# Kernel tuning notes

Hardware: AMD Instinct MI355X
Metric: run time of the kernel (lower is better)

The kernel has to match this reference:

```python
import jax, jax.numpy as jnp
import numpy as np

EMBED_DIM = 2048
HEAD_DIM = 128            # __init__ head_dim arg
HALF = HEAD_DIM // 2      # internal self.head_dim = 64
NH2 = EMBED_DIM // HALF   # 32 q/k heads
H = NH2 // 2              # 16 differential heads
DEPTH = 12
LAMBDA_INIT = 0.8 - 0.6 * float(np.exp(-0.3 * DEPTH))
SCALING = HEAD_DIM ** (-0.5)   # source divides scores by this (== *sqrt(head_dim))
BATCH, SEQ = 1, 2048
EPS = 1e-5


def setup_inputs() -> dict:
    key = jax.random.key(0)
    ks = jax.random.split(key, 10)
    wstd = 0.25 / float(np.sqrt(EMBED_DIM))  # keep logits moderate despite *sqrt(head_dim)
    return {
        "x": jax.random.normal(ks[0], (BATCH, SEQ, EMBED_DIM), jnp.float32),
        "wq": jax.random.normal(ks[1], (EMBED_DIM, EMBED_DIM), jnp.float32) * wstd,
        "wk": jax.random.normal(ks[2], (EMBED_DIM, EMBED_DIM), jnp.float32) * wstd,
        "wv": jax.random.normal(ks[3], (EMBED_DIM, EMBED_DIM), jnp.float32) * wstd,
        "wout": jax.random.normal(ks[4], (EMBED_DIM, EMBED_DIM), jnp.float32) * wstd,
        "lambda_q1": jax.random.normal(ks[5], (HALF,), jnp.float32) * 0.1,
        "lambda_q2": jax.random.normal(ks[6], (HALF,), jnp.float32) * 0.1,
        "lambda_k1": jax.random.normal(ks[7], (HALF,), jnp.float32) * 0.1,
        "lambda_k2": jax.random.normal(ks[8], (HALF,), jnp.float32) * 0.1,
        "subln_weight": jnp.ones((2 * HALF,), jnp.float32),
    }


def _rope_tables(t, dim):
    # precompute_freqs_cis: freqs = 1/theta^(arange(0,dim,2)/dim); angles = outer(t, freqs)
    inv = 1.0 / (10000.0 ** (np.arange(0, dim, 2)[: dim // 2].astype(np.float64) / dim))
    ang = np.outer(np.arange(t), inv)
    return jnp.asarray(np.cos(ang), jnp.float32), jnp.asarray(np.sin(ang), jnp.float32)


def _apply_rope(x, cos, sin):
    # x: [b, t, h, d]; interleaved (even, odd) pairs form complex numbers
    xr, xi = x[..., 0::2], x[..., 1::2]
    c = cos[None, :, None, :]
    s = sin[None, :, None, :]
    out = jnp.stack([xr * c - xi * s, xr * s + xi * c], axis=-1)
    return out.reshape(x.shape)


def reference(x, wq, wk, wv, wout, lambda_q1, lambda_q2, lambda_k1, lambda_k2, subln_weight):
    b, t, e = x.shape
    # nn.Linear(bias=False): y = x @ W^T
    q = (x @ wq.T).reshape(b, t, NH2, HALF)
    k = (x @ wk.T).reshape(b, t, NH2, HALF)
    v = (x @ wv.T).reshape(b, t, H, 2 * HALF)  # intended DIFF-attn layout
    cos, sin = _rope_tables(t, HALF)
    q = _apply_rope(q, cos, sin)
    k = _apply_rope(k, cos, sin)
    q = q.transpose(0, 2, 1, 3)  # [b, 2H, t, HALF]
    k = k.transpose(0, 2, 1, 3)
    v = v.transpose(0, 2, 1, 3)  # [b, H, t, 2*HALF]
    # source: attn_weights = qk / scaling  (scaling = head_dim**-0.5 -> multiply by sqrt(head_dim))
    scores = jnp.einsum('bhtd,bhsd->bhts', q, k) / SCALING
    # default attn_mask = triu(zeros) == all zeros -> no masking applied
    probs = jax.nn.softmax(scores, axis=-1)
    lam1 = jnp.exp(jnp.sum(lambda_q1 * lambda_k1))
    lam2 = jnp.exp(jnp.sum(lambda_q2 * lambda_k2))
    lam = lam1 - lam2 + LAMBDA_INIT
    probs = probs.reshape(b, H, 2, t, t)
    diff = probs[:, :, 0] - lam * probs[:, :, 1]        # [b, H, t, t]
    attn = jnp.einsum('bhts,bhsd->bhtd', diff, v)        # [b, H, t, 2*HALF]
    # RMSNorm(2*HALF, eps=1e-5)
    attn = attn * jax.lax.rsqrt(jnp.mean(attn * attn, axis=-1, keepdims=True) + EPS)
    attn = attn * subln_weight
    attn = attn.transpose(0, 2, 1, 3).reshape(b, t, e)
    return attn @ wout.T
```

## Files before the change

kernel.cpp:

```cpp
#include <hip/hip_runtime.h>
#include <math.h>

#define SEQ 2048
#define EMB 2048

typedef _Float16 f16;
typedef unsigned short ushort_t;
typedef __attribute__((ext_vector_type(2))) _Float16 f16x2;
typedef __attribute__((ext_vector_type(4))) _Float16 f16x4;
typedef __attribute__((ext_vector_type(8))) _Float16 f16x8;
typedef __attribute__((ext_vector_type(4))) float f32x4;
typedef __attribute__((ext_vector_type(8))) short bf16x8;
typedef __attribute__((ext_vector_type(4))) unsigned short us4;
typedef __attribute__((ext_vector_type(8))) unsigned short us8;

__device__ __forceinline__ void gload16(const void* g, void* l) {
  __builtin_amdgcn_global_load_lds((const __attribute__((address_space(1))) unsigned int*)g,
                                   (__attribute__((address_space(3))) unsigned int*)l, 16, 0, 0);
}

__device__ __forceinline__ ushort_t f32_to_bf16(float f) {
  unsigned int u = __builtin_bit_cast(unsigned int, f);
  u += 0x7FFFu + ((u >> 16) & 1u);
  return (ushort_t)(u >> 16);
}

__device__ __forceinline__ unsigned pack2_bf16(float a, float b) {
  unsigned ua = __builtin_bit_cast(unsigned, a) + 0x8000u;
  unsigned ub = __builtin_bit_cast(unsigned, b) + 0x8000u;
  return __builtin_amdgcn_perm(ub, ua, 0x07060302u);
}
__device__ __forceinline__ us4 pack4_bf16(float a, float b, float c, float d) {
  unsigned lo = pack2_bf16(a, b);
  unsigned hi = pack2_bf16(c, d);
  unsigned long long v = ((unsigned long long)hi << 32) | (unsigned long long)lo;
  return __builtin_bit_cast(us4, v);
}

__global__ __launch_bounds__(256) void cvt5_kernel(const float* __restrict__ i0,
                                                   const float* __restrict__ i1,
                                                   const float* __restrict__ i2,
                                                   const float* __restrict__ i3,
                                                   const float* __restrict__ i4,
                                                   f16* __restrict__ o0, f16* __restrict__ o1,
                                                   f16* __restrict__ o2, f16* __restrict__ o3,
                                                   f16* __restrict__ o4) {
  int b = blockIdx.x;
  int z = b >> 12;
  const float* in = (z == 0) ? i0 : (z == 1) ? i1 : (z == 2) ? i2 : (z == 3) ? i3 : i4;
  f16* out = (z == 0) ? o0 : (z == 1) ? o1 : (z == 2) ? o2 : (z == 3) ? o3 : o4;
  int i = ((b & 4095) * 256 + threadIdx.x) * 4;
  f32x4 v = *(const f32x4*)(in + i);
  *(f16x4*)(out + i) = __builtin_convertvector(v, f16x4);
}

__global__ __launch_bounds__(256) void rope_table_kernel(float* __restrict__ cosT,
                                                         float* __restrict__ sinT) {
  int id = blockIdx.x * 256 + threadIdx.x;
  int t = id >> 5, i = id & 31;
  double inv = pow(10000.0, -(double)i / 32.0);
  double ang = (double)t * inv;
  cosT[id] = (float)cos(ang);
  sinT[id] = (float)sin(ang);
}

__global__ __launch_bounds__(256) void rope2_kernel(f16* __restrict__ q, f16* __restrict__ k,
                                                    const float* __restrict__ cosT,
                                                    const float* __restrict__ sinT) {
  f16* x = blockIdx.y ? k : q;
  const float scale = blockIdx.y ? 1.0f : 16.3222307f;
  int id = blockIdx.x * 256 + threadIdx.x;
  int i = id & 31;
  int nh2 = (id >> 5) & 31;
  int t = id >> 10;
  float c = cosT[(t << 5) + i], s = sinT[(t << 5) + i];
  int base = t * EMB + nh2 * 64 + 2 * i;
  f16x2 p = *(f16x2*)(x + base);
  float xr = (float)p.x, xi = (float)p.y;
  f16x2 o;
  o.x = (f16)((xr * c - xi * s) * scale);
  o.y = (f16)((xr * s + xi * c) * scale);
  *(f16x2*)(x + base) = o;
}

__global__ __launch_bounds__(256, 3) void proj_gemm_kernel(
    const f16* __restrict__ A, const f16* __restrict__ B0, const f16* __restrict__ B1,
    const f16* __restrict__ B2, f16* __restrict__ qout, f16* __restrict__ kout,
    ushort_t* __restrict__ vtout) {
  const int z = blockIdx.z;
  const f16* __restrict__ B = (z == 0) ? B0 : ((z == 1) ? B1 : B2);
  __shared__ f16 As[128 * 32];
  __shared__ f16 Bs[128 * 32];
  const int tid = threadIdx.x;
  const int wave = tid >> 6, lane = tid & 63;
  const int l16 = lane & 15, quad = lane >> 4;
  const int wm = (wave >> 1) << 6, wn = (wave & 1) << 6;
  const int bm = blockIdx.y << 7, bn = blockIdx.x << 7;

  const int swg = ((lane & 3) ^ ((lane >> 3) & 3)) * 8;
  const f16* Ag = A + (size_t)(bm + wave * 32 + (lane >> 2)) * EMB + swg;
  const f16* Bg = B + (size_t)(bn + wave * 32 + (lane >> 2)) * EMB + swg;
  f16* Asl = &As[wave * 1024 + lane * 8];
  f16* Bsl = &Bs[wave * 1024 + lane * 8];

  const int swr = (quad ^ ((l16 >> 1) & 3)) * 8;
  int aoff[4], boff[4];
#pragma unroll
  for (int i = 0; i < 4; i++) {
    aoff[i] = (wm + i * 16 + l16) * 32 + swr;
    boff[i] = (wn + i * 16 + l16) * 32 + swr;
  }

  f32x4 acc[4][4];
#pragma unroll
  for (int i = 0; i < 4; i++)
#pragma unroll
    for (int j = 0; j < 4; j++) acc[i][j] = (f32x4){0.f, 0.f, 0.f, 0.f};

  for (int k0 = 0; k0 < EMB; k0 += 32) {
    __syncthreads();
    gload16(Ag + k0, Asl);
    gload16(Ag + (size_t)16 * EMB + k0, Asl + 512);
    gload16(Bg + k0, Bsl);
    gload16(Bg + (size_t)16 * EMB + k0, Bsl + 512);
    __syncthreads();
    f16x8 af[4], bf[4];
#pragma unroll
    for (int mi = 0; mi < 4; mi++) af[mi] = *(const f16x8*)&As[aoff[mi]];
#pragma unroll
    for (int ni = 0; ni < 4; ni++) bf[ni] = *(const f16x8*)&Bs[boff[ni]];
#pragma unroll
    for (int mi = 0; mi < 4; mi++)
#pragma unroll
      for (int ni = 0; ni < 4; ni++)
        acc[mi][ni] = __builtin_amdgcn_mfma_f32_16x16x32_f16(af[mi], bf[ni], acc[mi][ni], 0, 0, 0);
  }

#pragma unroll
  for (int mi = 0; mi < 4; mi++) {
#pragma unroll
    for (int ni = 0; ni < 4; ni++) {
      int row0 = bm + wm + mi * 16 + quad * 4;
      int col = bn + wn + ni * 16 + l16;
      if (z == 2) {
        us4 o;
#pragma unroll
        for (int rg = 0; rg < 4; rg++) o[rg] = f32_to_bf16(acc[mi][ni][rg]);
        int hidx = col >> 7, d = col & 127, t = row0;
        size_t idx = ((size_t)((hidx * 64 + (t >> 5)) * 8 + (d >> 4))) * 512 +
                     (((t >> 3) & 3) * 16 + (d & 15)) * 8 + (t & 7);
        *(us4*)&vtout[idx] = o;
      } else {
        f16* Co = (z == 0) ? qout : kout;
#pragma unroll
        for (int rg = 0; rg < 4; rg++)
          Co[(size_t)(row0 + rg) * EMB + col] = (f16)acc[mi][ni][rg];
      }
    }
  }
}

__global__ __launch_bounds__(256, 2) void out_gemm_kernel(const f16* __restrict__ A,
                                                          const f16* __restrict__ B,
                                                          float* __restrict__ C) {
  __shared__ f16 As[128 * 32];
  __shared__ f16 Bs[64 * 32];
  const int tid = threadIdx.x;
  const int wave = tid >> 6, lane = tid & 63;
  const int l16 = lane & 15, quad = lane >> 4;
  const int wm = (wave >> 1) << 6, wn = (wave & 1) << 5;
  const int bm = blockIdx.y << 7, bn = blockIdx.x << 6;

  const int swg = ((lane & 3) ^ ((lane >> 3) & 3)) * 8;
  const f16* Ag = A + (size_t)(bm + wave * 32 + (lane >> 2)) * EMB + swg;
  const f16* Bg = B + (size_t)(bn + wave * 16 + (lane >> 2)) * EMB + swg;
  f16* Asl = &As[wave * 1024 + lane * 8];
  f16* Bsl = &Bs[wave * 512 + lane * 8];

  const int swr = (quad ^ ((l16 >> 1) & 3)) * 8;
  int aoff[4], boff[2];
#pragma unroll
  for (int i = 0; i < 4; i++) aoff[i] = (wm + i * 16 + l16) * 32 + swr;
#pragma unroll
  for (int i = 0; i < 2; i++) boff[i] = (wn + i * 16 + l16) * 32 + swr;

  f32x4 acc[4][2];
#pragma unroll
  for (int i = 0; i < 4; i++)
#pragma unroll
    for (int j = 0; j < 2; j++) acc[i][j] = (f32x4){0.f, 0.f, 0.f, 0.f};

  for (int k0 = 0; k0 < EMB; k0 += 32) {
    __syncthreads();
    gload16(Ag + k0, Asl);
    gload16(Ag + (size_t)16 * EMB + k0, Asl + 512);
    gload16(Bg + k0, Bsl);
    __syncthreads();
    f16x8 af[4], bf[2];
#pragma unroll
    for (int mi = 0; mi < 4; mi++) af[mi] = *(const f16x8*)&As[aoff[mi]];
#pragma unroll
    for (int ni = 0; ni < 2; ni++) bf[ni] = *(const f16x8*)&Bs[boff[ni]];
#pragma unroll
    for (int mi = 0; mi < 4; mi++)
#pragma unroll
      for (int ni = 0; ni < 2; ni++)
        acc[mi][ni] = __builtin_amdgcn_mfma_f32_16x16x32_f16(af[mi], bf[ni], acc[mi][ni], 0, 0, 0);
  }

#pragma unroll
  for (int mi = 0; mi < 4; mi++) {
#pragma unroll
    for (int ni = 0; ni < 2; ni++) {
      int row0 = bm + wm + mi * 16 + quad * 4;
      int col = bn + wn + ni * 16 + l16;
#pragma unroll
      for (int rg = 0; rg < 4; rg++)
        C[(size_t)(row0 + rg) * EMB + col] = acc[mi][ni][rg];
    }
  }
}

__global__ __launch_bounds__(256, 2) void diff_attn_v4(
    const f16* __restrict__ qb, const f16* __restrict__ kb, const ushort_t* __restrict__ vbT,
    const float* __restrict__ lq1, const float* __restrict__ lq2,
    const float* __restrict__ lk1, const float* __restrict__ lk2,
    const float* __restrict__ subw, f16* __restrict__ attnb) {
  const int h = blockIdx.x;
  const int qblk = blockIdx.y;
  const int tid = threadIdx.x;
  const int wave = tid >> 6, lane = tid & 63;
  const int l16 = lane & 15, quad = lane >> 4;
  const int hh = wave >> 1, qs = wave & 1;

  __shared__ f16 Ks[2][8192];
  __shared__ ushort_t Vt[2][8192];
  __shared__ ushort_t Ps[4][2][2][512];

  const int qrow0 = qblk * 64 + qs * 32;
  f16x8 qf[2][2];
#pragma unroll
  for (int nt = 0; nt < 2; nt++)
#pragma unroll
    for (int kt = 0; kt < 2; kt++)
      qf[nt][kt] = *(const f16x8*)(qb + (size_t)(qrow0 + nt * 16 + l16) * EMB + h * 128 +
                                   hh * 64 + kt * 32 + quad * 8);

  f32x4 O[8][2];
#pragma unroll
  for (int mt = 0; mt < 8; mt++)
#pragma unroll
    for (int nt = 0; nt < 2; nt++) O[mt][nt] = (f32x4){0.f, 0.f, 0.f, 0.f};
  float lsum[2] = {0.f, 0.f};

  const f16* kgp = kb + (size_t)(wave * 16 + (lane >> 2)) * EMB + h * 128 + (lane & 3) * 32;
  int koff[4];
#pragma unroll
  for (int j = 0; j < 4; j++) {
    int Tk = ((lane & 3) >> 1) * 8 + ((lane & 3) & 1) * 4 + wave;
    koff[j] = Tk * 512 + (j * 16 + (lane >> 2)) * 8;
  }
  const ushort_t* vgp = vbT + ((size_t)h << 18) + (size_t)(wave * 4) * 512 + lane * 8;
  const int vo0 = (wave * 4) * 512 + lane * 8;

  {
    f16x8 kreg[4];
    us8 vreg[4];
#pragma unroll
    for (int j = 0; j < 4; j++) kreg[j] = *(const f16x8*)(kgp + j * 8);
#pragma unroll
    for (int j = 0; j < 4; j++) vreg[j] = *(const us8*)(vgp + j * 512);
#pragma unroll
    for (int j = 0; j < 4; j++) *(f16x8*)&Ks[0][koff[j]] = kreg[j];
#pragma unroll
    for (int j = 0; j < 4; j++) *(us8*)&Vt[0][vo0 + j * 512] = vreg[j];
    __syncthreads();
  }

  auto step = [&](const f16* KsC, const ushort_t* VtC, f16* KsN, ushort_t* VtN, int it) {
    const int nxt = (it + 1 < 32) ? (it + 1) : 0;
    f16x8 kreg[4];
    us8 vreg[4];
#pragma unroll
    for (int j = 0; j < 4; j++)
      kreg[j] = *(const f16x8*)(kgp + (size_t)(nxt * 64) * EMB + j * 8);
#pragma unroll
    for (int j = 0; j < 4; j++) vreg[j] = *(const us8*)(vgp + nxt * 8192 + j * 512);

#pragma unroll
    for (int mt = 0; mt < 4; mt++) {
      f16x8 ka0 = *(const f16x8*)&KsC[(hh * 8 + mt) * 512 + lane * 8];
      f16x8 ka1 = *(const f16x8*)&KsC[(hh * 8 + 4 + mt) * 512 + lane * 8];
#pragma unroll
      for (int nt = 0; nt < 2; nt++) {
        f32x4 c = (f32x4){0.f, 0.f, 0.f, 0.f};
        c = __builtin_amdgcn_mfma_f32_16x16x32_f16(ka0, qf[nt][0], c, 0, 0, 0);
        c = __builtin_amdgcn_mfma_f32_16x16x32_f16(ka1, qf[nt][1], c, 0, 0, 0);
        float p0 = __builtin_exp2f(c[0] - 28.8539008f);
        float p1 = __builtin_exp2f(c[1] - 28.8539008f);
        float p2 = __builtin_exp2f(c[2] - 28.8539008f);
        float p3 = __builtin_exp2f(c[3] - 28.8539008f);
        lsum[nt] += (p0 + p1) + (p2 + p3);
        us4 pb = pack4_bf16(p0, p1, p2, p3);
        int poff = (((mt & 1) * 2 + (quad >> 1)) * 16 + l16) * 8 + (quad & 1) * 4;
        *(us4*)&Ps[wave][nt][mt >> 1][poff] = pb;
      }
    }

#pragma unroll
    for (int kk = 0; kk < 2; kk++) {
      bf16x8 pf0 = *(const bf16x8*)&Ps[wave][0][kk][lane * 8];
      bf16x8 pf1 = *(const bf16x8*)&Ps[wave][1][kk][lane * 8];
#pragma unroll
      for (int mt = 0; mt < 8; mt++) {
        bf16x8 va = *(const bf16x8*)&VtC[(kk * 8 + mt) * 512 + lane * 8];
        O[mt][0] = __builtin_amdgcn_mfma_f32_16x16x32_bf16(va, pf0, O[mt][0], 0, 0, 0);
        O[mt][1] = __builtin_amdgcn_mfma_f32_16x16x32_bf16(va, pf1, O[mt][1], 0, 0, 0);
      }
    }

#pragma unroll
    for (int j = 0; j < 4; j++) *(f16x8*)&KsN[koff[j]] = kreg[j];
#pragma unroll
    for (int j = 0; j < 4; j++) *(us8*)&VtN[vo0 + j * 512] = vreg[j];
    __syncthreads();
  };

  for (int it = 0; it < 32; it += 2) {
    step(Ks[0], Vt[0], Ks[1], Vt[1], it);
    step(Ks[1], Vt[1], Ks[0], Vt[0], it + 1);
  }

  float d1 = 0.f, d2 = 0.f;
  for (int i = 0; i < 64; i++) {
    d1 += lq1[i] * lk1[i];
    d2 += lq2[i] * lk2[i];
  }
  const float lam = __expf(d1) - __expf(d2) + 0.783605767f;

  float inv[2];
#pragma unroll
  for (int nt = 0; nt < 2; nt++) {
    float s = lsum[nt];
    s += __shfl_xor(s, 16);
    s += __shfl_xor(s, 32);
    inv[nt] = (hh == 0) ? (1.f / s) : (lam / s);
  }

  float* Obuf = (float*)&Ks[0][0];
  if (hh == 1) {
#pragma unroll
    for (int mt = 0; mt < 8; mt++)
#pragma unroll
      for (int nt = 0; nt < 2; nt++) {
        f32x4 v = O[mt][nt] * inv[nt];
        *(f32x4*)&Obuf[((qs * 2 + nt) * 8 + mt) * 256 + lane * 4] = v;
      }
  }
  __syncthreads();
  if (hh == 0) {
    f32x4 swv[8];
#pragma unroll
    for (int mt = 0; mt < 8; mt++) swv[mt] = *(const f32x4*)(subw + mt * 16 + quad * 4);
#pragma unroll
    for (int nt = 0; nt < 2; nt++) {
      float a[8][4];
      float ms = 0.f;
#pragma unroll
      for (int mt = 0; mt < 8; mt++) {
        f32x4 o1 = *(const f32x4*)&Obuf[((qs * 2 + nt) * 8 + mt) * 256 + lane * 4];
#pragma unroll
        for (int rg = 0; rg < 4; rg++) {
          float v = O[mt][nt][rg] * inv[nt] - o1[rg];
          a[mt][rg] = v;
          ms += v * v;
        }
      }
      ms += __shfl_xor(ms, 16);
      ms += __shfl_xor(ms, 32);
      const float rms = rsqrtf(ms * (1.f / 128.f) + 1e-5f);
      const int t_g = qrow0 + nt * 16 + l16;
#pragma unroll
      for (int mt = 0; mt < 8; mt++) {
        f16x4 o;
#pragma unroll
        for (int rg = 0; rg < 4; rg++) o[rg] = (f16)(a[mt][rg] * rms * swv[mt][rg]);
        *(f16x4*)(attnb + (size_t)t_g * EMB + h * 128 + mt * 16 + quad * 4) = o;
      }
    }
  }
}

extern "C" void kernel_launch(void* const* d_in, const int* in_sizes, int n_in,
                              void* d_out, int out_size, void* d_ws, size_t ws_size,
                              hipStream_t stream) {
  const float* x    = (const float*)d_in[0];
  const float* wq   = (const float*)d_in[1];
  const float* wk   = (const float*)d_in[2];
  const float* wv   = (const float*)d_in[3];
  const float* wout = (const float*)d_in[4];
  const float* lq1  = (const float*)d_in[5];
  const float* lq2  = (const float*)d_in[6];
  const float* lk1  = (const float*)d_in[7];
  const float* lk2  = (const float*)d_in[8];
  const float* subw = (const float*)d_in[9];
  float* out = (float*)d_out;

  char* ws = (char*)d_ws;
  const size_t MB = 1024 * 1024;
  f16* xb    = (f16*)(ws + 0 * MB);
  f16* wqb   = (f16*)(ws + 8 * MB);
  f16* wkb   = (f16*)(ws + 16 * MB);
  f16* wvb   = (f16*)(ws + 24 * MB);
  f16* woutb = (f16*)(ws + 32 * MB);
  f16* qb    = (f16*)(ws + 40 * MB);
  f16* kb    = (f16*)(ws + 48 * MB);
  ushort_t* vbT = (ushort_t*)(ws + 56 * MB);
  f16* attnb = (f16*)(ws + 64 * MB);
  float* cosT = (float*)(ws + 72 * MB);
  float* sinT = (float*)(ws + 72 * MB + 262144);

  dim3 b256(256);
  cvt5_kernel<<<5 * 4096, b256, 0, stream>>>(x, wq, wk, wv, wout, xb, wqb, wkb, wvb, woutb);
  rope_table_kernel<<<256, b256, 0, stream>>>(cosT, sinT);

  proj_gemm_kernel<<<dim3(16, 16, 3), b256, 0, stream>>>(xb, wqb, wkb, wvb, qb, kb, vbT);

  rope2_kernel<<<dim3(8192, 2), b256, 0, stream>>>(qb, kb, cosT, sinT);

  diff_attn_v4<<<dim3(16, 32), b256, 0, stream>>>(qb, kb, vbT, lq1, lq2, lk1, lk2, subw, attnb);

  out_gemm_kernel<<<dim3(32, 16), b256, 0, stream>>>(attnb, woutb, out);
}
```

Measured before the change: 318.1 us.

## Double attention block to 8 waves, each owning 16 query rows

The differential attention kernel now runs 512 threads (8 waves) per block instead of 256. Each wave handles 16 query rows rather than 32. Half the waves stage K tiles and half stage V tiles, so each thread does half the global loads. The softmax offset is folded into the MFMA accumulator initialisation. The aim is more waves in flight to hide latency and lower register pressure per wave, at the cost of re-reading the shared K/V tiles from LDS twice as often per query row.

After: 310.7 us. 1.02x faster.

```diff
diff --git a/kernel.cpp b/kernel.cpp
--- a/kernel.cpp
+++ b/kernel.cpp
@@ -221,7 +221,7 @@
   }
 }
 
-__global__ __launch_bounds__(256, 2) void diff_attn_v4(
+__global__ __launch_bounds__(512, 4) void diff_attn_v5(
     const f16* __restrict__ qb, const f16* __restrict__ kb, const ushort_t* __restrict__ vbT,
     const float* __restrict__ lq1, const float* __restrict__ lq2,
     const float* __restrict__ lk1, const float* __restrict__ lk2,
@@ -231,104 +231,92 @@
   const int tid = threadIdx.x;
   const int wave = tid >> 6, lane = tid & 63;
   const int l16 = lane & 15, quad = lane >> 4;
-  const int hh = wave >> 1, qs = wave & 1;
+  const int hh = wave >> 2, qs = wave & 3;
 
   __shared__ f16 Ks[2][8192];
   __shared__ ushort_t Vt[2][8192];
-  __shared__ ushort_t Ps[4][2][2][512];
-
-  const int qrow0 = qblk * 64 + qs * 32;
-  f16x8 qf[2][2];
-#pragma unroll
-  for (int nt = 0; nt < 2; nt++)
-#pragma unroll
-    for (int kt = 0; kt < 2; kt++)
-      qf[nt][kt] = *(const f16x8*)(qb + (size_t)(qrow0 + nt * 16 + l16) * EMB + h * 128 +
-                                   hh * 64 + kt * 32 + quad * 8);
-
-  f32x4 O[8][2];
-#pragma unroll
-  for (int mt = 0; mt < 8; mt++)
-#pragma unroll
-    for (int nt = 0; nt < 2; nt++) O[mt][nt] = (f32x4){0.f, 0.f, 0.f, 0.f};
-  float lsum[2] = {0.f, 0.f};
-
-  const f16* kgp = kb + (size_t)(wave * 16 + (lane >> 2)) * EMB + h * 128 + (lane & 3) * 32;
-  int koff[4];
-#pragma unroll
-  for (int j = 0; j < 4; j++) {
-    int Tk = ((lane & 3) >> 1) * 8 + ((lane & 3) & 1) * 4 + wave;
-    koff[j] = Tk * 512 + (j * 16 + (lane >> 2)) * 8;
-  }
-  const ushort_t* vgp = vbT + ((size_t)h << 18) + (size_t)(wave * 4) * 512 + lane * 8;
-  const int vo0 = (wave * 4) * 512 + lane * 8;
+  __shared__ ushort_t Ps[8][2][512];
+
+  const int qrow0 = qblk * 64 + qs * 16;
+  f16x8 qf[2];
+#pragma unroll
+  for (int kt = 0; kt < 2; kt++)
+    qf[kt] = *(const f16x8*)(qb + (size_t)(qrow0 + l16) * EMB + h * 128 + hh * 64 + kt * 32 +
+                             quad * 8);
+
+  f32x4 O[8];
+#pragma unroll
+  for (int mt = 0; mt < 8; mt++) O[mt] = (f32x4){0.f, 0.f, 0.f, 0.f};
+  float lsum = 0.f;
+
+  const bool isK = (wave < 4);
+  const int sw = wave & 3;
+  const ushort_t* sg =
+      isK ? (const ushort_t*)(kb + (size_t)(sw * 16 + (lane >> 2)) * EMB + h * 128 +
+                              (lane & 3) * 8)
+          : vbT + ((size_t)h << 18) + sw * 2048 + lane * 8;
+  const int gchunk = isK ? 32 : 512;
+  const size_t gstep = isK ? (size_t)64 * EMB : 8192;
+  int soff[4];
+#pragma unroll
+  for (int j = 0; j < 4; j++)
+    soff[j] = isK ? (((j >> 1) * 8 + (j & 1) * 4 + sw) * 512 +
+                     ((lane & 3) * 16 + (lane >> 2)) * 8)
+                  : (sw * 2048 + j * 512 + lane * 8);
+  ushort_t* sb[2] = {isK ? (ushort_t*)&Ks[0][0] : &Vt[0][0],
+                     isK ? (ushort_t*)&Ks[1][0] : &Vt[1][0]};
 
   {
-    f16x8 kreg[4];
-    us8 vreg[4];
-#pragma unroll
-    for (int j = 0; j < 4; j++) kreg[j] = *(const f16x8*)(kgp + j * 8);
-#pragma unroll
-    for (int j = 0; j < 4; j++) vreg[j] = *(const us8*)(vgp + j * 512);
-#pragma unroll
-    for (int j = 0; j < 4; j++) *(f16x8*)&Ks[0][koff[j]] = kreg[j];
-#pragma unroll
-    for (int j = 0; j < 4; j++) *(us8*)&Vt[0][vo0 + j * 512] = vreg[j];
-    __syncthreads();
-  }
-
-  auto step = [&](const f16* KsC, const ushort_t* VtC, f16* KsN, ushort_t* VtN, int it) {
+    us8 sreg[4];
+#pragma unroll
+    for (int j = 0; j < 4; j++) sreg[j] = *(const us8*)(sg + j * gchunk);
+#pragma unroll
+    for (int j = 0; j < 4; j++) *(us8*)&sb[0][soff[j]] = sreg[j];
+    __syncthreads();
+  }
+
+  auto step = [&](const f16* KsC, const ushort_t* VtC, ushort_t* sbN, int it) {
     const int nxt = (it + 1 < 32) ? (it + 1) : 0;
-    f16x8 kreg[4];
-    us8 vreg[4];
+    us8 sreg[4];
 #pragma unroll
     for (int j = 0; j < 4; j++)
-      kreg[j] = *(const f16x8*)(kgp + (size_t)(nxt * 64) * EMB + j * 8);
-#pragma unroll
-    for (int j = 0; j < 4; j++) vreg[j] = *(const us8*)(vgp + nxt * 8192 + j * 512);
+      sreg[j] = *(const us8*)(sg + (size_t)nxt * gstep + j * gchunk);
 
 #pragma unroll
     for (int mt = 0; mt < 4; mt++) {
       f16x8 ka0 = *(const f16x8*)&KsC[(hh * 8 + mt) * 512 + lane * 8];
       f16x8 ka1 = *(const f16x8*)&KsC[(hh * 8 + 4 + mt) * 512 + lane * 8];
-#pragma unroll
-      for (int nt = 0; nt < 2; nt++) {
-        f32x4 c = (f32x4){0.f, 0.f, 0.f, 0.f};
-        c = __builtin_amdgcn_mfma_f32_16x16x32_f16(ka0, qf[nt][0], c, 0, 0, 0);
-        c = __builtin_amdgcn_mfma_f32_16x16x32_f16(ka1, qf[nt][1], c, 0, 0, 0);
-        float p0 = __builtin_exp2f(c[0] - 28.8539008f);
-        float p1 = __builtin_exp2f(c[1] - 28.8539008f);
-        float p2 = __builtin_exp2f(c[2] - 28.8539008f);
-        float p3 = __builtin_exp2f(c[3] - 28.8539008f);
-        lsum[nt] += (p0 + p1) + (p2 + p3);
-        us4 pb = pack4_bf16(p0, p1, p2, p3);
-        int poff = (((mt & 1) * 2 + (quad >> 1)) * 16 + l16) * 8 + (quad & 1) * 4;
-        *(us4*)&Ps[wave][nt][mt >> 1][poff] = pb;
-      }
+      f32x4 c = (f32x4){-28.8539008f, -28.8539008f, -28.8539008f, -28.8539008f};
+      c = __builtin_amdgcn_mfma_f32_16x16x32_f16(ka0, qf[0], c, 0, 0, 0);
+      c = __builtin_amdgcn_mfma_f32_16x16x32_f16(ka1, qf[1], c, 0, 0, 0);
+      float p0 = __builtin_exp2f(c[0]);
+      float p1 = __builtin_exp2f(c[1]);
+      float p2 = __builtin_exp2f(c[2]);
+      float p3 = __builtin_exp2f(c[3]);
+      lsum += (p0 + p1) + (p2 + p3);
+      us4 pb = pack4_bf16(p0, p1, p2, p3);
+      int poff = (((mt & 1) * 2 + (quad >> 1)) * 16 + l16) * 8 + (quad & 1) * 4;
+      *(us4*)&Ps[wave][mt >> 1][poff] = pb;
     }
 
 #pragma unroll
     for (int kk = 0; kk < 2; kk++) {
-      bf16x8 pf0 = *(const bf16x8*)&Ps[wave][0][kk][lane * 8];
-      bf16x8 pf1 = *(const bf16x8*)&Ps[wave][1][kk][lane * 8];
+      bf16x8 pf = *(const bf16x8*)&Ps[wave][kk][lane * 8];
 #pragma unroll
       for (int mt = 0; mt < 8; mt++) {
         bf16x8 va = *(const bf16x8*)&VtC[(kk * 8 + mt) * 512 + lane * 8];
-        O[mt][0] = __builtin_amdgcn_mfma_f32_16x16x32_bf16(va, pf0, O[mt][0], 0, 0, 0);
-        O[mt][1] = __builtin_amdgcn_mfma_f32_16x16x32_bf16(va, pf1, O[mt][1], 0, 0, 0);
+        O[mt] = __builtin_amdgcn_mfma_f32_16x16x32_bf16(va, pf, O[mt], 0, 0, 0);
       }
     }
 
 #pragma unroll
-    for (int j = 0; j < 4; j++) *(f16x8*)&KsN[koff[j]] = kreg[j];
-#pragma unroll
-    for (int j = 0; j < 4; j++) *(us8*)&VtN[vo0 + j * 512] = vreg[j];
+    for (int j = 0; j < 4; j++) *(us8*)&sbN[soff[j]] = sreg[j];
     __syncthreads();
   };
 
   for (int it = 0; it < 32; it += 2) {
-    step(Ks[0], Vt[0], Ks[1], Vt[1], it);
-    step(Ks[1], Vt[1], Ks[0], Vt[0], it + 1);
+    step(Ks[0], Vt[0], sb[1], it);
+    step(Ks[1], Vt[1], sb[0], it + 1);
   }
 
   float d1 = 0.f, d2 = 0.f;
@@ -338,55 +326,46 @@
   }
   const float lam = __expf(d1) - __expf(d2) + 0.783605767f;
 
-  float inv[2];
-#pragma unroll
-  for (int nt = 0; nt < 2; nt++) {
-    float s = lsum[nt];
-    s += __shfl_xor(s, 16);
-    s += __shfl_xor(s, 32);
-    inv[nt] = (hh == 0) ? (1.f / s) : (lam / s);
-  }
+  float s = lsum;
+  s += __shfl_xor(s, 16);
+  s += __shfl_xor(s, 32);
+  const float inv = (hh == 0) ? (1.f / s) : (lam / s);
 
   float* Obuf = (float*)&Ks[0][0];
   if (hh == 1) {
 #pragma unroll
-    for (int mt = 0; mt < 8; mt++)
-#pragma unroll
-      for (int nt = 0; nt < 2; nt++) {
-        f32x4 v = O[mt][nt] * inv[nt];
-        *(f32x4*)&Obuf[((qs * 2 + nt) * 8 + mt) * 256 + lane * 4] = v;
-      }
+    for (int mt = 0; mt < 8; mt++) {
+      f32x4 v = O[mt] * inv;
+      *(f32x4*)&Obuf[(qs * 8 + mt) * 256 + lane * 4] = v;
+    }
   }
   __syncthreads();
   if (hh == 0) {
     f32x4 swv[8];
 #pragma unroll
     for (int mt = 0; mt < 8; mt++) swv[mt] = *(const f32x4*)(subw + mt * 16 + quad * 4);
-#pragma unroll
-    for (int nt = 0; nt < 2; nt++) {
-      float a[8][4];
-      float ms = 0.f;
-#pragma unroll
-      for (int mt = 0; mt < 8; mt++) {
-        f32x4 o1 = *(const f32x4*)&Obuf[((qs * 2 + nt) * 8 + mt) * 256 + lane * 4];
-#pragma unroll
-        for (int rg = 0; rg < 4; rg++) {
-          float v = O[mt][nt][rg] * inv[nt] - o1[rg];
-          a[mt][rg] = v;
-          ms += v * v;
-        }
+    float a[8][4];
+    float ms = 0.f;
+#pragma unroll
+    for (int mt = 0; mt < 8; mt++) {
+      f32x4 o1 = *(const f32x4*)&Obuf[(qs * 8 + mt) * 256 + lane * 4];
+#pragma unroll
+      for (int rg = 0; rg < 4; rg++) {
+        float v = O[mt][rg] * inv - o1[rg];
+        a[mt][rg] = v;
+        ms += v * v;
       }
-      ms += __shfl_xor(ms, 16);
-      ms += __shfl_xor(ms, 32);
-      const float rms = rsqrtf(ms * (1.f / 128.f) + 1e-5f);
-      const int t_g = qrow0 + nt * 16 + l16;
-#pragma unroll
-      for (int mt = 0; mt < 8; mt++) {
-        f16x4 o;
-#pragma unroll
-        for (int rg = 0; rg < 4; rg++) o[rg] = (f16)(a[mt][rg] * rms * swv[mt][rg]);
-        *(f16x4*)(attnb + (size_t)t_g * EMB + h * 128 + mt * 16 + quad * 4) = o;
-      }
+    }
+    ms += __shfl_xor(ms, 16);
+    ms += __shfl_xor(ms, 32);
+    const float rms = rsqrtf(ms * (1.f / 128.f) + 1e-5f);
+    const int t_g = qrow0 + l16;
+#pragma unroll
+    for (int mt = 0; mt < 8; mt++) {
+      f16x4 o;
+#pragma unroll
+      for (int rg = 0; rg < 4; rg++) o[rg] = (f16)(a[mt][rg] * rms * swv[mt][rg]);
+      *(f16x4*)(attnb + (size_t)t_g * EMB + h * 128 + mt * 16 + quad * 4) = o;
     }
   }
 }
@@ -428,7 +407,8 @@
 
   rope2_kernel<<<dim3(8192, 2), b256, 0, stream>>>(qb, kb, cosT, sinT);
 
-  diff_attn_v4<<<dim3(16, 32), b256, 0, stream>>>(qb, kb, vbT, lq1, lq2, lk1, lk2, subw, attnb);
+  diff_attn_v5<<<dim3(16, 32), dim3(512), 0, stream>>>(qb, kb, vbT, lq1, lq2, lk1, lk2, subw,
+                                                       attnb);
 
   out_gemm_kernel<<<dim3(32, 16), b256, 0, stream>>>(attnb, woutb, out);
 }
```
